# Kernel optimization log

Hardware: AMD Instinct MI355X
Metric: run time of the kernel (lower is better)

## Reference

```python
import jax, jax.numpy as jnp
import numpy as np

NUM_GROUPS = 64      # number of distinct gt instance ids per image
PULL_WEIGHT = 1.0
PUSH_WEIGHT = 1.0
LOSS_WEIGHT = 1.0
EPS = 1e-6


def setup_inputs() -> dict:
    key = jax.random.key(0)
    k1, k2, k3 = jax.random.split(key, 3)
    B, N, D = 8, 500000, 8
    pred = jax.random.normal(k1, (B, N, D), dtype=jnp.float32)
    gt_inds = jax.random.randint(k2, (B, N), 0, NUM_GROUPS)
    anchor_inds = jax.random.randint(k3, (B, N), 0, 3)
    return {"pred": pred, "gt_inds": gt_inds, "anchor_inds": anchor_inds}


def _single_tag_loss(pred, gt):
    # pred: [N, D], gt: [N] int group ids in [0, NUM_GROUPS)
    N, D = pred.shape
    ones = jnp.ones((N,), pred.dtype)
    counts = jax.ops.segment_sum(ones, gt, num_segments=NUM_GROUPS)        # [G]
    sums = jax.ops.segment_sum(pred, gt, num_segments=NUM_GROUPS)          # [G, D]
    safe_counts = jnp.maximum(counts, 1.0)
    means = sums / safe_counts[:, None]                                    # per-group tag mean
    # pull: per-group mean over all elements of (group - mean)^2
    sq = ((pred - means[gt]) ** 2).sum(-1)                                 # [N]
    sumsq = jax.ops.segment_sum(sq, gt, num_segments=NUM_GROUPS)           # [G]
    present = counts > 0
    pull_g = jnp.where(present, sumsq / (safe_counts * D), 0.0)
    num = present.sum().astype(pred.dtype)
    pull = pull_g.sum() / (num + EPS)
    # push: pairwise exp(-||tag_i - tag_j||^2), masking absent groups
    d2 = ((means[:, None, :] - means[None, :, :]) ** 2).sum(-1)            # [G, G]
    m = present.astype(pred.dtype)
    push = (jnp.exp(-d2) * (m[:, None] * m[None, :])).sum() - num
    push = push / ((num - 1.0) * num + EPS) * 0.5
    return push * PUSH_WEIGHT + pull * PULL_WEIGHT


def reference(pred, gt_inds, anchor_inds):
    # group_anchor=False path: per-image single_tag_loss, averaged over images,
    # then scaled by loss_weight (reduction='mean' of a scalar is identity).
    per_img = jax.vmap(_single_tag_loss)(pred, gt_inds)                    # [B]
    return per_img.mean() * LOSS_WEIGHT
```

## Files before the change

### kernel.cpp

```cpp
#include <hip/hip_runtime.h>

#define GROUPS 64
#define DIMS 8
#define ACCW 10
#define LSTRIDE 11
#define BPI 128
#define BLK 256
#define NIMG 8
#define SCALE 262144.0f
#define INV_SCALE (1.0f / 262144.0f)

__global__ void k_zero(unsigned long long* p, int n) {
    int i = blockIdx.x * blockDim.x + threadIdx.x;
    if (i < n) p[i] = 0ull;
}

__global__ __launch_bounds__(BLK) void k_accum(const float* __restrict__ pred,
                                               const int* __restrict__ gt,
                                               unsigned long long* __restrict__ gacc,
                                               int N) {
    __shared__ int acc[4][GROUPS * LSTRIDE];
    const int tid = threadIdx.x;
    const int wave = tid >> 6;
    const int b = blockIdx.y;
    for (int i = tid; i < 4 * GROUPS * LSTRIDE; i += BLK) ((int*)acc)[i] = 0;
    __syncthreads();

    const float4* pb = (const float4*)(pred + (size_t)b * N * DIMS);
    const int* gb = gt + (size_t)b * N;
    for (int idx = blockIdx.x * BLK + tid; idx < N; idx += BPI * BLK) {
        int g = gb[idx];
        float4 p0 = pb[2 * idx];
        float4 p1 = pb[2 * idx + 1];
        int* a = &acc[wave][g * LSTRIDE];
        atomicAdd(a + 0, __float2int_rn(p0.x * SCALE));
        atomicAdd(a + 1, __float2int_rn(p0.y * SCALE));
        atomicAdd(a + 2, __float2int_rn(p0.z * SCALE));
        atomicAdd(a + 3, __float2int_rn(p0.w * SCALE));
        atomicAdd(a + 4, __float2int_rn(p1.x * SCALE));
        atomicAdd(a + 5, __float2int_rn(p1.y * SCALE));
        atomicAdd(a + 6, __float2int_rn(p1.z * SCALE));
        atomicAdd(a + 7, __float2int_rn(p1.w * SCALE));
        float ssq = p0.x*p0.x + p0.y*p0.y + p0.z*p0.z + p0.w*p0.w
                  + p1.x*p1.x + p1.y*p1.y + p1.z*p1.z + p1.w*p1.w;
        atomicAdd(a + 8, __float2int_rn(ssq * SCALE));
        atomicAdd(a + 9, 1);
    }
    __syncthreads();

    for (int i = tid; i < GROUPS * ACCW; i += BLK) {
        int g = i / ACCW, k = i % ACCW;
        long long v = (long long)acc[0][g * LSTRIDE + k]
                    + (long long)acc[1][g * LSTRIDE + k]
                    + (long long)acc[2][g * LSTRIDE + k]
                    + (long long)acc[3][g * LSTRIDE + k];
        atomicAdd(&gacc[(b * GROUPS + g) * ACCW + k], (unsigned long long)v);
    }
}

__global__ __launch_bounds__(512) void k_final(const unsigned long long* __restrict__ gacc,
                                               float* __restrict__ out) {
    __shared__ float sm[NIMG][GROUPS][DIMS + 1];
    __shared__ float lossArr[NIMG];
    const int tid = threadIdx.x;
    const int b = tid >> 6;
    const int g = tid & 63;

    const unsigned long long* ga = gacc + (b * GROUPS + g) * ACCW;
    float c = (float)(long long)ga[9];
    float ssq = (float)(long long)ga[8] * INV_SCALE;
    float safe = fmaxf(c, 1.f);
    float m[DIMS];
    float msq = 0.f;
    for (int d = 0; d < DIMS; ++d) {
        m[d] = ((float)(long long)ga[d] * INV_SCALE) / safe;
        sm[b][g][d] = m[d];
        msq += m[d] * m[d];
    }
    bool present = c > 0.f;
    sm[b][g][DIMS] = present ? 1.f : 0.f;

    float sumsq = ssq - c * msq;
    float pull_g = present ? sumsq / (safe * (float)DIMS) : 0.f;

    unsigned long long mask = __ballot(present);
    float num = (float)__popcll(mask);

    float pull = pull_g;
    for (int off = 32; off; off >>= 1) pull += __shfl_xor(pull, off);

    __syncthreads();

    float pg = 0.f;
    if (present) {
        for (int j = 0; j < GROUPS; ++j) {
            float pm = sm[b][j][DIMS];
            float d2 = 0.f;
            for (int d = 0; d < DIMS; ++d) {
                float t = m[d] - sm[b][j][d];
                d2 += t * t;
            }
            pg += pm * expf(-d2);
        }
    }
    for (int off = 32; off; off >>= 1) pg += __shfl_xor(pg, off);

    if (g == 0) {
        float push = (pg - num) / ((num - 1.f) * num + 1e-6f) * 0.5f;
        float pl = pull / (num + 1e-6f);
        lossArr[b] = push + pl;
    }
    __syncthreads();

    if (tid == 0) {
        float s = 0.f;
        for (int i = 0; i < NIMG; ++i) s += lossArr[i];
        out[0] = s * (1.f / (float)NIMG);
    }
}

extern "C" void kernel_launch(void* const* d_in, const int* in_sizes, int n_in,
                              void* d_out, int out_size, void* d_ws, size_t ws_size,
                              hipStream_t stream) {
    const float* pred = (const float*)d_in[0];
    const int* gt = (const int*)d_in[1];
    const int N = in_sizes[1] / NIMG;

    unsigned long long* gacc = (unsigned long long*)d_ws;
    const int accN = NIMG * GROUPS * ACCW;

    k_zero<<<(accN + 255) / 256, 256, 0, stream>>>(gacc, accN);
    dim3 grid(BPI, NIMG);
    k_accum<<<grid, BLK, 0, stream>>>(pred, gt, gacc, N);
    k_final<<<1, 512, 0, stream>>>(gacc, (float*)d_out);
}
```

Before: 43.74 us.

## Pack fixed-point sums into 64-bit LDS atomics and fuse finalization via last-block ticket

Each pair of per-dimension fixed-point values is packed into one 64-bit LDS atomic using a magic-number bias trick, and the sum of squares is packed with the count. This cuts LDS atomics per element from ten to five and spreads them across 16 shared copies instead of 4 to reduce contention. The separate zero and final kernels are replaced by a memset plus a last-block ticket that computes the loss inside the accumulation kernel, removing one launch. The bias correction depends on the per-copy count, and 23-bit fields can overflow if a copy sees too many elements or values are large.

```diff
diff --git a/kernel.cpp b/kernel.cpp
--- a/kernel.cpp
+++ b/kernel.cpp
@@ -3,118 +3,141 @@
 #define GROUPS 64
 #define DIMS 8
 #define ACCW 10
-#define LSTRIDE 11
+#define COPIES 16
+#define GSTRIDE 5
 #define BPI 128
 #define BLK 256
 #define NIMG 8
 #define SCALE 262144.0f
 #define INV_SCALE (1.0f / 262144.0f)
+#define MAGICF 12582912.0f
 
-__global__ void k_zero(unsigned long long* p, int n) {
-    int i = blockIdx.x * blockDim.x + threadIdx.x;
-    if (i < n) p[i] = 0ull;
+__device__ __forceinline__ unsigned int fieldOf(float x) {
+    return __float_as_uint(fmaf(x, SCALE, MAGICF)) & 0x007FFFFFu;
 }
 
 __global__ __launch_bounds__(BLK) void k_accum(const float* __restrict__ pred,
                                                const int* __restrict__ gt,
                                                unsigned long long* __restrict__ gacc,
+                                               unsigned long long* __restrict__ ticket,
+                                               float* __restrict__ out,
                                                int N) {
-    __shared__ int acc[4][GROUPS * LSTRIDE];
+    __shared__ unsigned long long accw[COPIES][GROUPS * GSTRIDE];
+    __shared__ int isLast;
     const int tid = threadIdx.x;
-    const int wave = tid >> 6;
     const int b = blockIdx.y;
-    for (int i = tid; i < 4 * GROUPS * LSTRIDE; i += BLK) ((int*)acc)[i] = 0;
+
+    for (int i = tid; i < COPIES * GROUPS * GSTRIDE; i += BLK)
+        ((unsigned long long*)accw)[i] = 0ull;
     __syncthreads();
 
     const float4* pb = (const float4*)(pred + (size_t)b * N * DIMS);
     const int* gb = gt + (size_t)b * N;
+    unsigned long long* myacc = &accw[(tid >> 2) & (COPIES - 1)][0];
+
     for (int idx = blockIdx.x * BLK + tid; idx < N; idx += BPI * BLK) {
         int g = gb[idx];
         float4 p0 = pb[2 * idx];
         float4 p1 = pb[2 * idx + 1];
-        int* a = &acc[wave][g * LSTRIDE];
-        atomicAdd(a + 0, __float2int_rn(p0.x * SCALE));
-        atomicAdd(a + 1, __float2int_rn(p0.y * SCALE));
-        atomicAdd(a + 2, __float2int_rn(p0.z * SCALE));
-        atomicAdd(a + 3, __float2int_rn(p0.w * SCALE));
-        atomicAdd(a + 4, __float2int_rn(p1.x * SCALE));
-        atomicAdd(a + 5, __float2int_rn(p1.y * SCALE));
-        atomicAdd(a + 6, __float2int_rn(p1.z * SCALE));
-        atomicAdd(a + 7, __float2int_rn(p1.w * SCALE));
+        unsigned long long* a = myacc + g * GSTRIDE;
+        atomicAdd(a + 0, (unsigned long long)fieldOf(p0.x) | ((unsigned long long)fieldOf(p0.y) << 32));
+        atomicAdd(a + 1, (unsigned long long)fieldOf(p0.z) | ((unsigned long long)fieldOf(p0.w) << 32));
+        atomicAdd(a + 2, (unsigned long long)fieldOf(p1.x) | ((unsigned long long)fieldOf(p1.y) << 32));
+        atomicAdd(a + 3, (unsigned long long)fieldOf(p1.z) | ((unsigned long long)fieldOf(p1.w) << 32));
         float ssq = p0.x*p0.x + p0.y*p0.y + p0.z*p0.z + p0.w*p0.w
                   + p1.x*p1.x + p1.y*p1.y + p1.z*p1.z + p1.w*p1.w;
-        atomicAdd(a + 8, __float2int_rn(ssq * SCALE));
-        atomicAdd(a + 9, 1);
+        unsigned int si = (unsigned int)__float2int_rn(ssq * SCALE);
+        atomicAdd(a + 4, (unsigned long long)si | (1ull << 32));
     }
     __syncthreads();
 
     for (int i = tid; i < GROUPS * ACCW; i += BLK) {
         int g = i / ACCW, k = i % ACCW;
-        long long v = (long long)acc[0][g * LSTRIDE + k]
-                    + (long long)acc[1][g * LSTRIDE + k]
-                    + (long long)acc[2][g * LSTRIDE + k]
-                    + (long long)acc[3][g * LSTRIDE + k];
+        long long v = 0;
+        if (k < 8) {
+            int w = k >> 1, hi = k & 1;
+            for (int c = 0; c < COPIES; ++c) {
+                unsigned long long pw = accw[c][g * GSTRIDE + w];
+                unsigned long long cw = accw[c][g * GSTRIDE + 4];
+                unsigned int f = hi ? (unsigned int)(pw >> 32) : (unsigned int)pw;
+                v += (long long)f - (long long)((cw >> 32) << 22);
+            }
+        } else if (k == 8) {
+            for (int c = 0; c < COPIES; ++c)
+                v += (long long)(unsigned int)accw[c][g * GSTRIDE + 4];
+        } else {
+            for (int c = 0; c < COPIES; ++c)
+                v += (long long)(accw[c][g * GSTRIDE + 4] >> 32);
+        }
         atomicAdd(&gacc[(b * GROUPS + g) * ACCW + k], (unsigned long long)v);
     }
-}
 
-__global__ __launch_bounds__(512) void k_final(const unsigned long long* __restrict__ gacc,
-                                               float* __restrict__ out) {
-    __shared__ float sm[NIMG][GROUPS][DIMS + 1];
-    __shared__ float lossArr[NIMG];
-    const int tid = threadIdx.x;
-    const int b = tid >> 6;
+    __threadfence();
+    __syncthreads();
+    if (tid == 0) {
+        unsigned long long t = atomicAdd(ticket, 1ull);
+        isLast = (t == (unsigned long long)(gridDim.x * gridDim.y) - 1ull) ? 1 : 0;
+    }
+    __syncthreads();
+    if (!isLast) return;
+    __threadfence();
+
+    float* smf = (float*)&accw[0][0];
+    float* lossF = smf + NIMG * GROUPS * (DIMS + 1);
+    const int wv = tid >> 6;
     const int g = tid & 63;
+    for (int ib = wv; ib < NIMG; ib += 4) {
+        unsigned long long ga[ACCW];
+        const unsigned long long* gp = gacc + (ib * GROUPS + g) * ACCW;
+        for (int k = 0; k < ACCW; ++k)
+            ga[k] = __hip_atomic_load(gp + k, __ATOMIC_RELAXED, __HIP_MEMORY_SCOPE_AGENT);
+        float c = (float)(long long)ga[9];
+        float ssq = (float)(long long)ga[8] * INV_SCALE;
+        float safe = fmaxf(c, 1.f);
+        float m[DIMS];
+        float msq = 0.f;
+        float* row = smf + (ib * GROUPS + g) * (DIMS + 1);
+        for (int d = 0; d < DIMS; ++d) {
+            m[d] = ((float)(long long)ga[d] * INV_SCALE) / safe;
+            row[d] = m[d];
+            msq += m[d] * m[d];
+        }
+        bool present = c > 0.f;
+        row[DIMS] = present ? 1.f : 0.f;
 
-    const unsigned long long* ga = gacc + (b * GROUPS + g) * ACCW;
-    float c = (float)(long long)ga[9];
-    float ssq = (float)(long long)ga[8] * INV_SCALE;
-    float safe = fmaxf(c, 1.f);
-    float m[DIMS];
-    float msq = 0.f;
-    for (int d = 0; d < DIMS; ++d) {
-        m[d] = ((float)(long long)ga[d] * INV_SCALE) / safe;
-        sm[b][g][d] = m[d];
-        msq += m[d] * m[d];
-    }
-    bool present = c > 0.f;
-    sm[b][g][DIMS] = present ? 1.f : 0.f;
+        float sumsq = ssq - c * msq;
+        float pull_g = present ? sumsq / (safe * (float)DIMS) : 0.f;
 
-    float sumsq = ssq - c * msq;
-    float pull_g = present ? sumsq / (safe * (float)DIMS) : 0.f;
+        unsigned long long mask = __ballot(present);
+        float num = (float)__popcll(mask);
 
-    unsigned long long mask = __ballot(present);
-    float num = (float)__popcll(mask);
+        float pull = pull_g;
+        for (int off = 32; off; off >>= 1) pull += __shfl_xor(pull, off);
 
-    float pull = pull_g;
-    for (int off = 32; off; off >>= 1) pull += __shfl_xor(pull, off);
+        float pg = 0.f;
+        if (present) {
+            for (int j = 0; j < GROUPS; ++j) {
+                const float* rj = smf + (ib * GROUPS + j) * (DIMS + 1);
+                float pm = rj[DIMS];
+                float d2 = 0.f;
+                for (int d = 0; d < DIMS; ++d) {
+                    float t2 = m[d] - rj[d];
+                    d2 += t2 * t2;
+                }
+                pg += pm * expf(-d2);
+            }
+        }
+        for (int off = 32; off; off >>= 1) pg += __shfl_xor(pg, off);
 
-    __syncthreads();
-
-    float pg = 0.f;
-    if (present) {
-        for (int j = 0; j < GROUPS; ++j) {
-            float pm = sm[b][j][DIMS];
-            float d2 = 0.f;
-            for (int d = 0; d < DIMS; ++d) {
-                float t = m[d] - sm[b][j][d];
-                d2 += t * t;
-            }
-            pg += pm * expf(-d2);
+        if (g == 0) {
+            float push = (pg - num) / ((num - 1.f) * num + 1e-6f) * 0.5f;
+            lossF[ib] = push + pull / (num + 1e-6f);
         }
     }
-    for (int off = 32; off; off >>= 1) pg += __shfl_xor(pg, off);
-
-    if (g == 0) {
-        float push = (pg - num) / ((num - 1.f) * num + 1e-6f) * 0.5f;
-        float pl = pull / (num + 1e-6f);
-        lossArr[b] = push + pl;
-    }
     __syncthreads();
-
     if (tid == 0) {
         float s = 0.f;
-        for (int i = 0; i < NIMG; ++i) s += lossArr[i];
+        for (int i = 0; i < NIMG; ++i) s += lossF[i];
         out[0] = s * (1.f / (float)NIMG);
     }
 }
@@ -127,10 +150,10 @@
     const int N = in_sizes[1] / NIMG;
 
     unsigned long long* gacc = (unsigned long long*)d_ws;
-    const int accN = NIMG * GROUPS * ACCW;
+    unsigned long long* ticket = gacc + NIMG * GROUPS * ACCW;
 
-    k_zero<<<(accN + 255) / 256, 256, 0, stream>>>(gacc, accN);
+    hipMemsetAsync(d_ws, 0, (NIMG * GROUPS * ACCW + 1) * sizeof(unsigned long long), stream);
+
     dim3 grid(BPI, NIMG);
-    k_accum<<<grid, BLK, 0, stream>>>(pred, gt, gacc, N);
-    k_final<<<1, 512, 0, stream>>>(gacc, (float*)d_out);
+    k_accum<<<grid, BLK, 0, stream>>>(pred, gt, gacc, ticket, (float*)d_out, N);
 }
```

Result: slower. 113.8 us (+160.1%).

## Fuse final loss reduction into accumulate kernel via last-block ticket

Applied to the files above, without the earlier changes.

Removes the separate finalize kernel: each block takes an atomic ticket after its global atomics, and the last block to arrive computes the per-image pull/push losses and writes the output. The zero kernel is replaced by hipMemsetAsync, which also clears the ticket. This cuts kernel launch count and inter-kernel gaps. In exchange the accumulate kernel uses more shared memory, and the last block runs the 8-image tail with only 256 threads, two images per wave.

```diff
diff --git a/kernel.cpp b/kernel.cpp
--- a/kernel.cpp
+++ b/kernel.cpp
@@ -10,16 +10,17 @@
 #define SCALE 262144.0f
 #define INV_SCALE (1.0f / 262144.0f)
 
-__global__ void k_zero(unsigned long long* p, int n) {
-    int i = blockIdx.x * blockDim.x + threadIdx.x;
-    if (i < n) p[i] = 0ull;
-}
-
 __global__ __launch_bounds__(BLK) void k_accum(const float* __restrict__ pred,
                                                const int* __restrict__ gt,
                                                unsigned long long* __restrict__ gacc,
+                                               unsigned long long* __restrict__ ticket,
+                                               float* __restrict__ out,
                                                int N) {
     __shared__ int acc[4][GROUPS * LSTRIDE];
+    __shared__ float smf[NIMG][GROUPS][DIMS + 1];
+    __shared__ float lossArr[NIMG];
+    __shared__ int isLast;
+
     const int tid = threadIdx.x;
     const int wave = tid >> 6;
     const int b = blockIdx.y;
@@ -56,62 +57,65 @@
                     + (long long)acc[3][g * LSTRIDE + k];
         atomicAdd(&gacc[(b * GROUPS + g) * ACCW + k], (unsigned long long)v);
     }
-}
-
-__global__ __launch_bounds__(512) void k_final(const unsigned long long* __restrict__ gacc,
-                                               float* __restrict__ out) {
-    __shared__ float sm[NIMG][GROUPS][DIMS + 1];
-    __shared__ float lossArr[NIMG];
-    const int tid = threadIdx.x;
-    const int b = tid >> 6;
-    const int g = tid & 63;
-
-    const unsigned long long* ga = gacc + (b * GROUPS + g) * ACCW;
-    float c = (float)(long long)ga[9];
-    float ssq = (float)(long long)ga[8] * INV_SCALE;
-    float safe = fmaxf(c, 1.f);
-    float m[DIMS];
-    float msq = 0.f;
-    for (int d = 0; d < DIMS; ++d) {
-        m[d] = ((float)(long long)ga[d] * INV_SCALE) / safe;
-        sm[b][g][d] = m[d];
-        msq += m[d] * m[d];
-    }
-    bool present = c > 0.f;
-    sm[b][g][DIMS] = present ? 1.f : 0.f;
-
-    float sumsq = ssq - c * msq;
-    float pull_g = present ? sumsq / (safe * (float)DIMS) : 0.f;
-
-    unsigned long long mask = __ballot(present);
-    float num = (float)__popcll(mask);
-
-    float pull = pull_g;
-    for (int off = 32; off; off >>= 1) pull += __shfl_xor(pull, off);
 
     __syncthreads();
+    if (tid == 0) {
+        unsigned long long t = __hip_atomic_fetch_add(ticket, 1ull, __ATOMIC_ACQ_REL,
+                                                      __HIP_MEMORY_SCOPE_AGENT);
+        isLast = (t == (unsigned long long)(BPI * NIMG) - 1ull) ? 1 : 0;
+    }
+    __syncthreads();
+    if (!isLast) return;
 
-    float pg = 0.f;
-    if (present) {
-        for (int j = 0; j < GROUPS; ++j) {
-            float pm = sm[b][j][DIMS];
-            float d2 = 0.f;
-            for (int d = 0; d < DIMS; ++d) {
-                float t = m[d] - sm[b][j][d];
-                d2 += t * t;
+    const int wv = tid >> 6;
+    const int g = tid & 63;
+    for (int ib = wv; ib < NIMG; ib += 4) {
+        unsigned long long ga[ACCW];
+        const unsigned long long* gp = gacc + (ib * GROUPS + g) * ACCW;
+        for (int k = 0; k < ACCW; ++k)
+            ga[k] = __hip_atomic_load(gp + k, __ATOMIC_RELAXED, __HIP_MEMORY_SCOPE_AGENT);
+        float c = (float)(long long)ga[9];
+        float ssq = (float)(long long)ga[8] * INV_SCALE;
+        float safe = fmaxf(c, 1.f);
+        float m[DIMS];
+        float msq = 0.f;
+        for (int d = 0; d < DIMS; ++d) {
+            m[d] = ((float)(long long)ga[d] * INV_SCALE) / safe;
+            smf[ib][g][d] = m[d];
+            msq += m[d] * m[d];
+        }
+        bool present = c > 0.f;
+        smf[ib][g][DIMS] = present ? 1.f : 0.f;
+
+        float sumsq = ssq - c * msq;
+        float pull_g = present ? sumsq / (safe * (float)DIMS) : 0.f;
+
+        unsigned long long mask = __ballot(present);
+        float num = (float)__popcll(mask);
+
+        float pull = pull_g;
+        for (int off = 32; off; off >>= 1) pull += __shfl_xor(pull, off);
+
+        float pg = 0.f;
+        if (present) {
+            for (int j = 0; j < GROUPS; ++j) {
+                float pm = smf[ib][j][DIMS];
+                float d2 = 0.f;
+                for (int d = 0; d < DIMS; ++d) {
+                    float t2 = m[d] - smf[ib][j][d];
+                    d2 += t2 * t2;
+                }
+                pg += pm * expf(-d2);
             }
-            pg += pm * expf(-d2);
+        }
+        for (int off = 32; off; off >>= 1) pg += __shfl_xor(pg, off);
+
+        if (g == 0) {
+            float push = (pg - num) / ((num - 1.f) * num + 1e-6f) * 0.5f;
+            lossArr[ib] = push + pull / (num + 1e-6f);
         }
     }
-    for (int off = 32; off; off >>= 1) pg += __shfl_xor(pg, off);
-
-    if (g == 0) {
-        float push = (pg - num) / ((num - 1.f) * num + 1e-6f) * 0.5f;
-        float pl = pull / (num + 1e-6f);
-        lossArr[b] = push + pl;
-    }
     __syncthreads();
-
     if (tid == 0) {
         float s = 0.f;
         for (int i = 0; i < NIMG; ++i) s += lossArr[i];
@@ -127,10 +131,10 @@
     const int N = in_sizes[1] / NIMG;
 
     unsigned long long* gacc = (unsigned long long*)d_ws;
-    const int accN = NIMG * GROUPS * ACCW;
+    unsigned long long* ticket = gacc + NIMG * GROUPS * ACCW;
 
-    k_zero<<<(accN + 255) / 256, 256, 0, stream>>>(gacc, accN);
+    hipMemsetAsync(d_ws, 0, (NIMG * GROUPS * ACCW + 1) * sizeof(unsigned long long), stream);
+
     dim3 grid(BPI, NIMG);
-    k_accum<<<grid, BLK, 0, stream>>>(pred, gt, gacc, N);
-    k_final<<<1, 512, 0, stream>>>(gacc, (float*)d_out);
+    k_accum<<<grid, BLK, 0, stream>>>(pred, gt, gacc, ticket, (float*)d_out, N);
 }
```

After: 73.78 us. 1.69x slower.
